# Kernel tuning notes

Hardware: AMD Instinct MI355X
Metric: run time of the kernel (lower is better)

Reference implementation:

```python
import jax, jax.numpy as jnp
import numpy as np

EMBED = 2048
HEADS = 32
HEAD_DIM = EMBED // HEADS
ALPHA = 12.0
MAX_SEQ = 1024
GAMMA = -ALPHA / MAX_SEQ  # clipped softmax lower stretch
ETA = 1.0


def setup_inputs() -> dict:
    key = jax.random.key(0)
    ks = jax.random.split(key, 12)
    B, T, E, H, D = 4, 1024, EMBED, HEADS, HEAD_DIM
    s = 1.0 / np.sqrt(E)
    hidden_states = jax.random.normal(ks[0], (B, T, E), dtype=jnp.float32)
    # causal attention mask: True = attend
    causal = jnp.tril(jnp.ones((T, T), dtype=bool))
    attention_mask = jnp.broadcast_to(causal[None, None], (B, 1, T, T))
    Wq = jax.random.normal(ks[1], (E, E), dtype=jnp.float32) * s
    bq = jnp.zeros((E,), dtype=jnp.float32)
    Wk = jax.random.normal(ks[2], (E, E), dtype=jnp.float32) * s
    bk = jnp.zeros((E,), dtype=jnp.float32)
    Wv = jax.random.normal(ks[3], (E, E), dtype=jnp.float32) * s
    bv = jnp.zeros((E,), dtype=jnp.float32)
    Wo = jax.random.normal(ks[4], (E, E), dtype=jnp.float32) * s
    bo = jnp.zeros((E,), dtype=jnp.float32)
    gate_w = jax.random.normal(ks[5], (H, D), dtype=jnp.float32) * (1.0 / np.sqrt(D))
    gate_b = jnp.zeros((H,), dtype=jnp.float32)
    return {"hidden_states": hidden_states, "attention_mask": attention_mask,
            "Wq": Wq, "bq": bq, "Wk": Wk, "bk": bk, "Wv": Wv, "bv": bv,
            "Wo": Wo, "bo": bo, "gate_w": gate_w, "gate_b": gate_b}


def clipped_softmax(x, gamma, eta):
    p = jax.nn.softmax(x, axis=-1)
    return jnp.clip((eta - gamma) * p + gamma, 0.0, 1.0)


def reference(hidden_states, attention_mask, Wq, bq, Wk, bk, Wv, bv, Wo, bo, gate_w, gate_b):
    B, T, E = hidden_states.shape
    H, D = HEADS, HEAD_DIM
    scaling = D ** -0.5
    neg_min = jnp.finfo(hidden_states.dtype).min

    q = ((hidden_states @ Wq.T + bq) * scaling).reshape(B, T, H, D)
    k = (hidden_states @ Wk.T + bk).reshape(B, T, H, D)
    v = (hidden_states @ Wv.T + bv).reshape(B, T, H, D)

    # scores: [B,H,T,S]
    scores = jnp.einsum('bthd,bshd->bhts', q, k)
    mask_add = jnp.where(attention_mask, 0.0, neg_min)  # [B,1,T,S]
    scores = jnp.maximum(scores + mask_add, neg_min)

    probs = clipped_softmax(scores, GAMMA, ETA)

    attn_out = jnp.einsum('bhts,bshd->bhtd', probs, v)  # [B,H,T,D]

    # conditional_per_token gate: per-head Linear(head_dim -> 1), sigmoid
    x_heads = hidden_states.reshape(B, T, H, D)
    gate = jax.nn.sigmoid(jnp.einsum('bthd,hd->bht', x_heads, gate_w) + gate_b[None, :, None])
    attn_out = attn_out * gate[..., None]  # gate_scaling_factor = 1.0

    out = attn_out.transpose(0, 2, 1, 3).reshape(B, T, E)
    return out @ Wo.T + bo
```

## Files before the change

kernel.cpp:

```cpp
#include <hip/hip_runtime.h>
#include <hip/hip_bf16.h>

typedef unsigned short ushort_t;
using short8 = __attribute__((ext_vector_type(8))) short;
using f32x4  = __attribute__((ext_vector_type(4))) float;

constexpr int B_ = 4;
constexpr int T_ = 1024;
constexpr int E_ = 2048;
constexpr int H_ = 32;
constexpr int D_ = 64;
constexpr float GAMMA_  = -12.0f / 1024.0f;
constexpr float ONE_MG_ = 1.0f - GAMMA_;

__device__ __forceinline__ ushort_t f2bf(float f) {
  union { float f; unsigned int i; } x; x.f = f;
  unsigned int u = x.i;
  u += 0x7fffu + ((u >> 16) & 1u);
  return (ushort_t)(u >> 16);
}

__global__ __launch_bounds__(256) void f2bf_multi(
    const float* __restrict__ x,
    const float* __restrict__ Wq, const float* __restrict__ Wk,
    const float* __restrict__ Wv, const float* __restrict__ Wo,
    ushort_t* __restrict__ xb,
    ushort_t* __restrict__ wqb, ushort_t* __restrict__ wkb,
    ushort_t* __restrict__ wvb, ushort_t* __restrict__ wob) {
  const int i = blockIdx.x * 256 + threadIdx.x;
  const float* src; ushort_t* dst; int off;
  if (i < 2097152)      { src = x;  dst = xb;  off = i; }
  else if (i < 3145728) { src = Wq; dst = wqb; off = i - 2097152; }
  else if (i < 4194304) { src = Wk; dst = wkb; off = i - 3145728; }
  else if (i < 5242880) { src = Wv; dst = wvb; off = i - 4194304; }
  else                  { src = Wo; dst = wob; off = i - 5242880; }
  const float4 f = ((const float4*)src)[off];
  ushort4 u; u.x = f2bf(f.x); u.y = f2bf(f.y); u.z = f2bf(f.z); u.w = f2bf(f.w);
  ((ushort4*)dst)[off] = u;
}

__device__ __forceinline__ void gl_lds16(const ushort_t* g, ushort_t* l) {
  __builtin_amdgcn_global_load_lds(
      (const __attribute__((address_space(1))) void*)g,
      (__attribute__((address_space(3))) void*)l, 16, 0, 0);
}

__global__ __launch_bounds__(256) void gemm_qkv(
    const ushort_t* __restrict__ xb,
    const ushort_t* __restrict__ wq, const ushort_t* __restrict__ wk,
    const ushort_t* __restrict__ wv,
    const float* __restrict__ bq, const float* __restrict__ bk,
    const float* __restrict__ bv,
    ushort_t* __restrict__ qout, ushort_t* __restrict__ kout,
    ushort_t* __restrict__ vtout) {
  constexpr int K = 2048;
  __shared__ ushort_t As[128 * 32];
  __shared__ ushort_t Bs[128 * 32];
  const int which = blockIdx.x >> 4;
  const int colt  = blockIdx.x & 15;
  const ushort_t* Wt  = (which == 0) ? wq : (which == 1) ? wk : wv;
  const float*   bias = (which == 0) ? bq : (which == 1) ? bk : bv;
  const float    scale = (which == 0) ? 0.125f : 1.0f;

  const int tid = threadIdx.x;
  const int wave = tid >> 6, lane = tid & 63;
  const int lane15 = lane & 15, quad = lane >> 4;
  const int row0 = blockIdx.y * 128, col0 = colt * 128;
  const int srow = lane >> 2;
  const int scol = (lane & 3) * 8;
  const ushort_t* Ag0 = xb + (size_t)(row0 + wave * 32 + srow) * K + scol;
  const ushort_t* Ag1 = Ag0 + 16 * (size_t)K;
  const ushort_t* Bg0 = Wt + (size_t)(col0 + wave * 32 + srow) * K + scol;
  const ushort_t* Bg1 = Bg0 + 16 * (size_t)K;
  ushort_t* Al0 = &As[(wave * 32     ) * 32];
  ushort_t* Al1 = &As[(wave * 32 + 16) * 32];
  ushort_t* Bl0 = &Bs[(wave * 32     ) * 32];
  ushort_t* Bl1 = &Bs[(wave * 32 + 16) * 32];
  const int wr = wave >> 1, wc = wave & 1;
  const int q8 = quad * 8;

  f32x4 acc[4][4];
#pragma unroll
  for (int i = 0; i < 4; i++)
#pragma unroll
    for (int j = 0; j < 4; j++) acc[i][j] = (f32x4){0.f, 0.f, 0.f, 0.f};

  for (int k0 = 0; k0 < K; k0 += 32) {
    __syncthreads();
    gl_lds16(Ag0 + k0, Al0);
    gl_lds16(Ag1 + k0, Al1);
    gl_lds16(Bg0 + k0, Bl0);
    gl_lds16(Bg1 + k0, Bl1);
    __syncthreads();
    short8 a_f[4], b_f[4];
#pragma unroll
    for (int i = 0; i < 4; i++)
      a_f[i] = *(const short8*)&As[(wr * 64 + i * 16 + lane15) * 32 + q8];
#pragma unroll
    for (int j = 0; j < 4; j++)
      b_f[j] = *(const short8*)&Bs[(wc * 64 + j * 16 + lane15) * 32 + q8];
#pragma unroll
    for (int i = 0; i < 4; i++)
#pragma unroll
      for (int j = 0; j < 4; j++)
        acc[i][j] = __builtin_amdgcn_mfma_f32_16x16x32_bf16(
            a_f[i], b_f[j], acc[i][j], 0, 0, 0);
  }

  ushort_t* outp = (which == 0) ? qout : (which == 1) ? kout : vtout;
#pragma unroll
  for (int j = 0; j < 4; j++) {
    const int c = col0 + wc * 64 + j * 16 + lane15;
    const float bia = bias[c];
#pragma unroll
    for (int i = 0; i < 4; i++) {
#pragma unroll
      for (int reg = 0; reg < 4; reg++) {
        const int r = row0 + wr * 64 + i * 16 + quad * 4 + reg;
        const float val = (acc[i][j][reg] + bia) * scale;
        const int b = r >> 10, t = r & 1023, h = c >> 6, d = c & 63;
        if (which < 2)
          outp[(((size_t)(b * 32 + h)) * 1024 + t) * 64 + d] = f2bf(val);
        else
          outp[(((size_t)(b * 32 + h)) * 64 + d) * 1024 + t] = f2bf(val);
      }
    }
  }
}

__global__ __launch_bounds__(256) void gemm_out(
    const ushort_t* __restrict__ A, const ushort_t* __restrict__ Wt,
    const float* __restrict__ bias, float* __restrict__ Cout) {
  constexpr int K = 2048;
  __shared__ ushort_t As[128 * 32];
  __shared__ ushort_t Bs[128 * 32];
  const int tid = threadIdx.x;
  const int wave = tid >> 6, lane = tid & 63;
  const int lane15 = lane & 15, quad = lane >> 4;
  const int row0 = blockIdx.y * 128, col0 = blockIdx.x * 128;
  const int srow = lane >> 2;
  const int scol = (lane & 3) * 8;
  const ushort_t* Ag0 = A  + (size_t)(row0 + wave * 32 + srow) * K + scol;
  const ushort_t* Ag1 = Ag0 + 16 * (size_t)K;
  const ushort_t* Bg0 = Wt + (size_t)(col0 + wave * 32 + srow) * K + scol;
  const ushort_t* Bg1 = Bg0 + 16 * (size_t)K;
  ushort_t* Al0 = &As[(wave * 32     ) * 32];
  ushort_t* Al1 = &As[(wave * 32 + 16) * 32];
  ushort_t* Bl0 = &Bs[(wave * 32     ) * 32];
  ushort_t* Bl1 = &Bs[(wave * 32 + 16) * 32];
  const int wr = wave >> 1, wc = wave & 1;
  const int q8 = quad * 8;

  f32x4 acc[4][4];
#pragma unroll
  for (int i = 0; i < 4; i++)
#pragma unroll
    for (int j = 0; j < 4; j++) acc[i][j] = (f32x4){0.f, 0.f, 0.f, 0.f};

  for (int k0 = 0; k0 < K; k0 += 32) {
    __syncthreads();
    gl_lds16(Ag0 + k0, Al0);
    gl_lds16(Ag1 + k0, Al1);
    gl_lds16(Bg0 + k0, Bl0);
    gl_lds16(Bg1 + k0, Bl1);
    __syncthreads();
    short8 a_f[4], b_f[4];
#pragma unroll
    for (int i = 0; i < 4; i++)
      a_f[i] = *(const short8*)&As[(wr * 64 + i * 16 + lane15) * 32 + q8];
#pragma unroll
    for (int j = 0; j < 4; j++)
      b_f[j] = *(const short8*)&Bs[(wc * 64 + j * 16 + lane15) * 32 + q8];
#pragma unroll
    for (int i = 0; i < 4; i++)
#pragma unroll
      for (int j = 0; j < 4; j++)
        acc[i][j] = __builtin_amdgcn_mfma_f32_16x16x32_bf16(
            a_f[i], b_f[j], acc[i][j], 0, 0, 0);
  }

#pragma unroll
  for (int j = 0; j < 4; j++) {
    const int c = col0 + wc * 64 + j * 16 + lane15;
    const float bia = bias[c];
#pragma unroll
    for (int i = 0; i < 4; i++) {
#pragma unroll
      for (int reg = 0; reg < 4; reg++) {
        const int r = row0 + wr * 64 + i * 16 + quad * 4 + reg;
        Cout[(size_t)r * 2048 + c] = acc[i][j][reg] + bia;
      }
    }
  }
}

__global__ __launch_bounds__(256) void gates_kernel(
    const float* __restrict__ x, const float* __restrict__ gw,
    const float* __restrict__ gb, float* __restrict__ gates) {
  const int idx = blockIdx.x * 256 + threadIdx.x;
  const int h = idx & 31;
  const int bt = idx >> 5;
  const float* xp = x + (size_t)bt * E_ + h * D_;
  const float* wp = gw + h * D_;
  float s = 0.f;
#pragma unroll
  for (int d = 0; d < D_; d += 4) {
    const float4 xv = *(const float4*)&xp[d];
    const float4 wv = *(const float4*)&wp[d];
    s = fmaf(xv.x, wv.x, s); s = fmaf(xv.y, wv.y, s);
    s = fmaf(xv.z, wv.z, s); s = fmaf(xv.w, wv.w, s);
  }
  s += gb[h];
  gates[idx] = 1.0f / (1.0f + __expf(-s));
}

__global__ __launch_bounds__(256) void attn_mfma(
    const ushort_t* __restrict__ q, const ushort_t* __restrict__ k,
    const ushort_t* __restrict__ vt, const float* __restrict__ gates,
    ushort_t* __restrict__ attn_out) {
  __shared__ ushort_t Kt[64 * 72];
  __shared__ ushort_t Vt[64 * 72];
  __shared__ ushort_t Pb[4][16 * 72];

  const int tid = threadIdx.x;
  const int wave = tid >> 6, lane = tid & 63;
  const int l15 = lane & 15, quad = lane >> 4;
  const int bx = blockIdx.x;
  const int qt = 7 - (bx >> 7);
  const int bh = bx & 127;
  const int h = bh & 31, b = bh >> 5;
  const int t0 = qt * 128;
  const int qt8 = qt * 8;
  const ushort_t* qbase = q  + (size_t)bh * (T_ * D_);
  const ushort_t* kbase = k  + (size_t)bh * (T_ * D_);
  const ushort_t* vbase = vt + (size_t)bh * (D_ * T_);

  short8 qf[2][2];
#pragma unroll
  for (int s = 0; s < 2; s++) {
    const ushort_t* qp =
        qbase + (size_t)(t0 + s * 64 + wave * 16 + l15) * 64 + quad * 8;
    qf[s][0] = *(const short8*)qp;
    qf[s][1] = *(const short8*)(qp + 32);
  }

  const int srow = tid >> 2;
  const int scol = (tid & 3) * 16;
  const int nkt = 2 * qt + 2;

  float l_part[2][4] = {};

  for (int kt = 0; kt < nkt; kt++) {
    __syncthreads();
    {
      const ushort_t* kg = &kbase[(size_t)(kt * 64 + srow) * 64 + scol];
      ushort_t* kl = &Kt[srow * 72 + scol];
      *(short8*)kl = *(const short8*)kg;
      *(short8*)(kl + 8) = *(const short8*)(kg + 8);
    }
    __syncthreads();
#pragma unroll
    for (int s = 0; s < 2; s++) {
      const int rb = qt8 + s * 4 + wave;
      if (kt * 4 > rb) continue;
      f32x4 sc[4];
#pragma unroll
      for (int j = 0; j < 4; j++) {
        const int cb = kt * 4 + j;
        if (cb > rb) {
          sc[j] = (f32x4){-3.0e38f, -3.0e38f, -3.0e38f, -3.0e38f};
          continue;
        }
        const ushort_t* kp = &Kt[(j * 16 + l15) * 72 + quad * 8];
        const short8 kf0 = *(const short8*)kp;
        const short8 kf1 = *(const short8*)(kp + 32);
        f32x4 z = (f32x4){0.f, 0.f, 0.f, 0.f};
        z = __builtin_amdgcn_mfma_f32_16x16x32_bf16(qf[s][0], kf0, z, 0, 0, 0);
        z = __builtin_amdgcn_mfma_f32_16x16x32_bf16(qf[s][1], kf1, z, 0, 0, 0);
        if (cb == rb) {
#pragma unroll
          for (int r = 0; r < 4; r++)
            if (l15 > quad * 4 + r) z[r] = -3.0e38f;
        }
        sc[j] = z;
      }
#pragma unroll
      for (int r = 0; r < 4; r++)
        l_part[s][r] += __expf(sc[0][r]) + __expf(sc[1][r]) +
                        __expf(sc[2][r]) + __expf(sc[3][r]);
    }
  }

  float c1[2][4];
#pragma unroll
  for (int s = 0; s < 2; s++)
#pragma unroll
    for (int r = 0; r < 4; r++) {
      float e = l_part[s][r];
      e += __shfl_xor(e, 1); e += __shfl_xor(e, 2);
      e += __shfl_xor(e, 4); e += __shfl_xor(e, 8);
      c1[s][r] = ONE_MG_ / e;
    }

  f32x4 acc[2][4];
#pragma unroll
  for (int s = 0; s < 2; s++)
#pragma unroll
    for (int jd = 0; jd < 4; jd++) acc[s][jd] = (f32x4){0.f, 0.f, 0.f, 0.f};

  for (int kt = 0; kt < nkt; kt++) {
    __syncthreads();
    {
      const ushort_t* kg = &kbase[(size_t)(kt * 64 + srow) * 64 + scol];
      ushort_t* kl = &Kt[srow * 72 + scol];
      *(short8*)kl = *(const short8*)kg;
      *(short8*)(kl + 8) = *(const short8*)(kg + 8);
      const ushort_t* vg = &vbase[(size_t)srow * 1024 + kt * 64 + scol];
      ushort_t* vl = &Vt[srow * 72 + scol];
      *(short8*)vl = *(const short8*)vg;
      *(short8*)(vl + 8) = *(const short8*)(vg + 8);
    }
    __syncthreads();
#pragma unroll
    for (int s = 0; s < 2; s++) {
      const int rb = qt8 + s * 4 + wave;
      if (kt * 4 > rb) continue;
      f32x4 sc[4];
#pragma unroll
      for (int j = 0; j < 4; j++) {
        const int cb = kt * 4 + j;
        if (cb > rb) {
          sc[j] = (f32x4){-3.0e38f, -3.0e38f, -3.0e38f, -3.0e38f};
          continue;
        }
        const ushort_t* kp = &Kt[(j * 16 + l15) * 72 + quad * 8];
        const short8 kf0 = *(const short8*)kp;
        const short8 kf1 = *(const short8*)(kp + 32);
        f32x4 z = (f32x4){0.f, 0.f, 0.f, 0.f};
        z = __builtin_amdgcn_mfma_f32_16x16x32_bf16(qf[s][0], kf0, z, 0, 0, 0);
        z = __builtin_amdgcn_mfma_f32_16x16x32_bf16(qf[s][1], kf1, z, 0, 0, 0);
        if (cb == rb) {
#pragma unroll
          for (int r = 0; r < 4; r++)
            if (l15 > quad * 4 + r) z[r] = -3.0e38f;
        }
        sc[j] = z;
      }
      ushort_t* pb = &Pb[wave][0];
#pragma unroll
      for (int j = 0; j < 4; j++) {
#pragma unroll
        for (int r = 0; r < 4; r++) {
          float p = fmaf(c1[s][r], __expf(sc[j][r]), GAMMA_);
          p = fminf(fmaxf(p, 0.f), 1.f);
          pb[(quad * 4 + r) * 72 + j * 16 + l15] = f2bf(p);
        }
      }
      const short8 pf0 = *(const short8*)&pb[l15 * 72 + quad * 8];
      const short8 pf1 = *(const short8*)&pb[l15 * 72 + 32 + quad * 8];
#pragma unroll
      for (int jd = 0; jd < 4; jd++) {
        const ushort_t* vp = &Vt[(jd * 16 + l15) * 72 + quad * 8];
        const short8 vf0 = *(const short8*)vp;
        const short8 vf1 = *(const short8*)(vp + 32);
        acc[s][jd] =
            __builtin_amdgcn_mfma_f32_16x16x32_bf16(pf0, vf0, acc[s][jd], 0, 0, 0);
        acc[s][jd] =
            __builtin_amdgcn_mfma_f32_16x16x32_bf16(pf1, vf1, acc[s][jd], 0, 0, 0);
      }
    }
  }

#pragma unroll
  for (int s = 0; s < 2; s++) {
#pragma unroll
    for (int r = 0; r < 4; r++) {
      const int t = t0 + s * 64 + wave * 16 + quad * 4 + r;
      const float g = gates[((size_t)b * T_ + t) * H_ + h];
      ushort_t* op = attn_out + ((size_t)b * T_ + t) * E_ + h * 64;
#pragma unroll
      for (int jd = 0; jd < 4; jd++)
        op[jd * 16 + l15] = f2bf(acc[s][jd][r] * g);
    }
  }
}

extern "C" void kernel_launch(void* const* d_in, const int* in_sizes, int n_in,
                              void* d_out, int out_size, void* d_ws, size_t ws_size,
                              hipStream_t stream) {
  (void)in_sizes; (void)n_in; (void)out_size; (void)ws_size;
  const float* x  = (const float*)d_in[0];
  const float* Wq = (const float*)d_in[2];
  const float* bq = (const float*)d_in[3];
  const float* Wk = (const float*)d_in[4];
  const float* bk = (const float*)d_in[5];
  const float* Wv = (const float*)d_in[6];
  const float* bv = (const float*)d_in[7];
  const float* Wo = (const float*)d_in[8];
  const float* bo = (const float*)d_in[9];
  const float* gw = (const float*)d_in[10];
  const float* gb = (const float*)d_in[11];
  float* out = (float*)d_out;

  char* W = (char*)d_ws;
  ushort_t* xb  = (ushort_t*)(W + 0);
  ushort_t* wqb = (ushort_t*)(W + 16777216);
  ushort_t* wkb = (ushort_t*)(W + 25165824);
  ushort_t* wvb = (ushort_t*)(W + 33554432);
  ushort_t* wob = (ushort_t*)(W + 41943040);
  ushort_t* qb  = (ushort_t*)(W + 50331648);
  ushort_t* kb  = (ushort_t*)(W + 67108864);
  ushort_t* vtb = (ushort_t*)(W + 83886080);
  ushort_t* ab  = (ushort_t*)(W + 100663296);
  float*    gts = (float*)(W + 117440512);

  f2bf_multi<<<24576, 256, 0, stream>>>(x, Wq, Wk, Wv, Wo,
                                        xb, wqb, wkb, wvb, wob);

  gemm_qkv<<<dim3(48, 32), 256, 0, stream>>>(xb, wqb, wkb, wvb,
                                             bq, bk, bv, qb, kb, vtb);
  gates_kernel<<<512, 256, 0, stream>>>(x, gw, gb, gts);
  attn_mfma<<<1024, 256, 0, stream>>>(qb, kb, vtb, gts, ab);
  gemm_out<<<dim3(16, 32), 256, 0, stream>>>(ab, wob, bo, out);
}
```

Before: 435.1 us.

## Replace QKV and output GEMMs with a pipelined 256x256 tile core

Both GEMMs move from a 128x128 tile with a single LDS buffer and two barriers per 32-wide k step to a shared 256x256 core with 8 waves. The core double-buffers 64-wide k slices in XOR-swizzled LDS and issues global-to-LDS loads for upcoming slices between four MFMA quadrant phases, using s_setprio and explicit vmcnt waits. It also remaps block indices to improve L2 reuse. The goal is to hide memory latency, cut LDS bank conflicts and raise MFMA utilisation. The trade-offs are far fewer blocks (128 for the output GEMM, which is under one full wave on the CU count), more register and LDS pressure, and more barriers per iteration.

Result: slower. 449.4 us (+3.3%).

```diff
diff --git a/kernel.cpp b/kernel.cpp
--- a/kernel.cpp
+++ b/kernel.cpp
@@ -45,7 +45,128 @@
       (__attribute__((address_space(3))) void*)l, 16, 0, 0);
 }
 
-__global__ __launch_bounds__(256) void gemm_qkv(
+
+__device__ __forceinline__ void stage_half(
+    const ushort_t* __restrict__ g, int grow0, int k0,
+    ushort_t* l, int wid, int lane) {
+  const int rl = lane >> 3;
+  const int c7 = (lane & 7) ^ rl;
+#pragma unroll
+  for (int q = 0; q < 2; q++) {
+    const ushort_t* src =
+        g + (size_t)(grow0 + (q * 8 + wid) * 8 + rl) * 2048 + k0 + c7 * 8;
+    gl_lds16(src, l + (q * 8 + wid) * 512);
+  }
+}
+
+__device__ __forceinline__ void ld_a(short8 (&a)[8], const ushort_t* base,
+                                     int wm, int l15, int sw0, int sw1) {
+#pragma unroll
+  for (int m = 0; m < 4; m++) {
+    const ushort_t* p = base + (wm * 64 + m * 16 + l15) * 64;
+    a[m * 2 + 0] = *(const short8*)(p + sw0);
+    a[m * 2 + 1] = *(const short8*)(p + sw1);
+  }
+}
+
+__device__ __forceinline__ void ld_b(short8 (&b)[4], const ushort_t* base,
+                                     int wn, int l15, int sw0, int sw1) {
+#pragma unroll
+  for (int n = 0; n < 2; n++) {
+    const ushort_t* p = base + (wn * 32 + n * 16 + l15) * 64;
+    b[n * 2 + 0] = *(const short8*)(p + sw0);
+    b[n * 2 + 1] = *(const short8*)(p + sw1);
+  }
+}
+
+template <int QM, int QN>
+__device__ __forceinline__ void mfma_phase(f32x4 (&acc)[8][4],
+                                           const short8 (&a)[8],
+                                           const short8 (&bfr)[4]) {
+#pragma unroll
+  for (int m = 0; m < 4; m++)
+#pragma unroll
+    for (int n = 0; n < 2; n++)
+#pragma unroll
+      for (int kc = 0; kc < 2; kc++)
+        acc[QM * 4 + m][QN * 2 + n] = __builtin_amdgcn_mfma_f32_16x16x32_bf16(
+            a[m * 2 + kc], bfr[n * 2 + kc], acc[QM * 4 + m][QN * 2 + n],
+            0, 0, 0);
+}
+
+#define GFENCE asm volatile("" ::: "memory")
+
+__device__ __forceinline__ void gemm256_core(
+    const ushort_t* __restrict__ Ag, const ushort_t* __restrict__ Bg,
+    const int row0, const int col0,
+    ushort_t (&lds)[2][2][2][8192], f32x4 (&acc)[8][4]) {
+  const int tid = threadIdx.x;
+  const int wid = tid >> 6, lane = tid & 63;
+  const int wm = wid >> 2, wn = wid & 3;
+  const int l15 = lane & 15, quad = lane >> 4;
+  const int sw0 = (quad * 8) ^ ((l15 & 7) << 3);
+  const int sw1 = (32 + quad * 8) ^ ((l15 & 7) << 3);
+
+#pragma unroll
+  for (int i = 0; i < 8; i++)
+#pragma unroll
+    for (int j = 0; j < 4; j++) acc[i][j] = (f32x4){0.f, 0.f, 0.f, 0.f};
+
+  short8 a[8], bfr[4];
+
+  stage_half(Ag, row0,       0,  &lds[0][0][0][0], wid, lane);
+  stage_half(Bg, col0 + 128, 0,  &lds[0][1][1][0], wid, lane);
+  stage_half(Ag, row0 + 128, 0,  &lds[0][0][1][0], wid, lane);
+  stage_half(Bg, col0,       0,  &lds[0][1][0][0], wid, lane);
+  stage_half(Ag, row0,       64, &lds[1][0][0][0], wid, lane);
+  stage_half(Bg, col0 + 128, 64, &lds[1][1][1][0], wid, lane);
+  stage_half(Ag, row0 + 128, 64, &lds[1][0][1][0], wid, lane);
+  asm volatile("s_waitcnt vmcnt(6)" ::: "memory");
+  __builtin_amdgcn_s_barrier();
+  GFENCE;
+
+  for (int t = 0; t < 32; ++t) {
+    const int buf = t & 1;
+    const int kf = (t + 2) * 64;
+    ld_a(a, &lds[buf][0][0][0], wm, l15, sw0, sw1);
+    ld_b(bfr, &lds[buf][1][0][0], wn, l15, sw0, sw1);
+    if (t + 1 < 32)
+      stage_half(Bg, col0, (t + 1) * 64, &lds[buf ^ 1][1][0][0], wid, lane);
+    GFENCE; __builtin_amdgcn_s_barrier(); GFENCE;
+    __builtin_amdgcn_s_setprio(1);
+    mfma_phase<0, 0>(acc, a, bfr);
+    __builtin_amdgcn_s_setprio(0);
+    GFENCE; __builtin_amdgcn_s_barrier(); GFENCE;
+    ld_b(bfr, &lds[buf][1][1][0], wn, l15, sw0, sw1);
+    if (t + 2 < 32)
+      stage_half(Ag, row0, kf, &lds[buf][0][0][0], wid, lane);
+    GFENCE; __builtin_amdgcn_s_barrier(); GFENCE;
+    __builtin_amdgcn_s_setprio(1);
+    mfma_phase<0, 1>(acc, a, bfr);
+    __builtin_amdgcn_s_setprio(0);
+    GFENCE; __builtin_amdgcn_s_barrier(); GFENCE;
+    ld_a(a, &lds[buf][0][1][0], wm, l15, sw0, sw1);
+    if (t + 2 < 32)
+      stage_half(Bg, col0 + 128, kf, &lds[buf][1][1][0], wid, lane);
+    GFENCE; __builtin_amdgcn_s_barrier(); GFENCE;
+    __builtin_amdgcn_s_setprio(1);
+    mfma_phase<1, 1>(acc, a, bfr);
+    __builtin_amdgcn_s_setprio(0);
+    GFENCE; __builtin_amdgcn_s_barrier(); GFENCE;
+    ld_b(bfr, &lds[buf][1][0][0], wn, l15, sw0, sw1);
+    if (t + 2 < 32)
+      stage_half(Ag, row0 + 128, kf, &lds[buf][0][1][0], wid, lane);
+    GFENCE; __builtin_amdgcn_s_barrier(); GFENCE;
+    __builtin_amdgcn_s_setprio(1);
+    mfma_phase<1, 0>(acc, a, bfr);
+    __builtin_amdgcn_s_setprio(0);
+    if (t < 30)       asm volatile("s_waitcnt vmcnt(6)" ::: "memory");
+    else if (t == 30) asm volatile("s_waitcnt vmcnt(0)" ::: "memory");
+    GFENCE; __builtin_amdgcn_s_barrier(); GFENCE;
+  }
+}
+
+__global__ __launch_bounds__(512, 2) void gemm_qkv256(
     const ushort_t* __restrict__ xb,
     const ushort_t* __restrict__ wq, const ushort_t* __restrict__ wk,
     const ushort_t* __restrict__ wv,
@@ -53,143 +174,73 @@
     const float* __restrict__ bv,
     ushort_t* __restrict__ qout, ushort_t* __restrict__ kout,
     ushort_t* __restrict__ vtout) {
-  constexpr int K = 2048;
-  __shared__ ushort_t As[128 * 32];
-  __shared__ ushort_t Bs[128 * 32];
-  const int which = blockIdx.x >> 4;
-  const int colt  = blockIdx.x & 15;
+  __shared__ ushort_t lds[2][2][2][8192];
+  const int g = blockIdx.x;
+  const int swz = (g & 7) * 48 + (g >> 3);
+  const int which = swz >> 7;
+  const int rem = swz & 127;
+  const int row0 = (rem & 15) * 256;
+  const int col0 = (rem >> 4) * 256;
   const ushort_t* Wt  = (which == 0) ? wq : (which == 1) ? wk : wv;
   const float*   bias = (which == 0) ? bq : (which == 1) ? bk : bv;
   const float    scale = (which == 0) ? 0.125f : 1.0f;
+  ushort_t* outp = (which == 0) ? qout : (which == 1) ? kout : vtout;
+
+  f32x4 acc[8][4];
+  gemm256_core(xb, Wt, row0, col0, lds, acc);
 
   const int tid = threadIdx.x;
-  const int wave = tid >> 6, lane = tid & 63;
-  const int lane15 = lane & 15, quad = lane >> 4;
-  const int row0 = blockIdx.y * 128, col0 = colt * 128;
-  const int srow = lane >> 2;
-  const int scol = (lane & 3) * 8;
-  const ushort_t* Ag0 = xb + (size_t)(row0 + wave * 32 + srow) * K + scol;
-  const ushort_t* Ag1 = Ag0 + 16 * (size_t)K;
-  const ushort_t* Bg0 = Wt + (size_t)(col0 + wave * 32 + srow) * K + scol;
-  const ushort_t* Bg1 = Bg0 + 16 * (size_t)K;
-  ushort_t* Al0 = &As[(wave * 32     ) * 32];
-  ushort_t* Al1 = &As[(wave * 32 + 16) * 32];
-  ushort_t* Bl0 = &Bs[(wave * 32     ) * 32];
-  ushort_t* Bl1 = &Bs[(wave * 32 + 16) * 32];
-  const int wr = wave >> 1, wc = wave & 1;
-  const int q8 = quad * 8;
-
-  f32x4 acc[4][4];
-#pragma unroll
-  for (int i = 0; i < 4; i++)
-#pragma unroll
-    for (int j = 0; j < 4; j++) acc[i][j] = (f32x4){0.f, 0.f, 0.f, 0.f};
-
-  for (int k0 = 0; k0 < K; k0 += 32) {
-    __syncthreads();
-    gl_lds16(Ag0 + k0, Al0);
-    gl_lds16(Ag1 + k0, Al1);
-    gl_lds16(Bg0 + k0, Bl0);
-    gl_lds16(Bg1 + k0, Bl1);
-    __syncthreads();
-    short8 a_f[4], b_f[4];
-#pragma unroll
-    for (int i = 0; i < 4; i++)
-      a_f[i] = *(const short8*)&As[(wr * 64 + i * 16 + lane15) * 32 + q8];
-#pragma unroll
-    for (int j = 0; j < 4; j++)
-      b_f[j] = *(const short8*)&Bs[(wc * 64 + j * 16 + lane15) * 32 + q8];
-#pragma unroll
-    for (int i = 0; i < 4; i++)
-#pragma unroll
-      for (int j = 0; j < 4; j++)
-        acc[i][j] = __builtin_amdgcn_mfma_f32_16x16x32_bf16(
-            a_f[i], b_f[j], acc[i][j], 0, 0, 0);
-  }
-
-  ushort_t* outp = (which == 0) ? qout : (which == 1) ? kout : vtout;
-#pragma unroll
-  for (int j = 0; j < 4; j++) {
-    const int c = col0 + wc * 64 + j * 16 + lane15;
-    const float bia = bias[c];
-#pragma unroll
-    for (int i = 0; i < 4; i++) {
+  const int wid = tid >> 6, lane = tid & 63;
+  const int wm = wid >> 2, wn = wid & 3;
+  const int l15 = lane & 15, quad = lane >> 4;
+#pragma unroll
+  for (int ai = 0; ai < 8; ai++) {
+    const int r0 = row0 + (ai >> 2) * 128 + wm * 64 + (ai & 3) * 16 + quad * 4;
+#pragma unroll
+    for (int aj = 0; aj < 4; aj++) {
+      const int c = col0 + (aj >> 1) * 128 + wn * 32 + (aj & 1) * 16 + l15;
+      const float bia = bias[c];
+      const int h = c >> 6, d = c & 63;
 #pragma unroll
       for (int reg = 0; reg < 4; reg++) {
-        const int r = row0 + wr * 64 + i * 16 + quad * 4 + reg;
-        const float val = (acc[i][j][reg] + bia) * scale;
-        const int b = r >> 10, t = r & 1023, h = c >> 6, d = c & 63;
+        const int rr = r0 + reg;
+        const float val = (acc[ai][aj][reg] + bia) * scale;
+        const int b = rr >> 10, tt = rr & 1023;
         if (which < 2)
-          outp[(((size_t)(b * 32 + h)) * 1024 + t) * 64 + d] = f2bf(val);
+          outp[(((size_t)(b * 32 + h)) * 1024 + tt) * 64 + d] = f2bf(val);
         else
-          outp[(((size_t)(b * 32 + h)) * 64 + d) * 1024 + t] = f2bf(val);
+          outp[(((size_t)(b * 32 + h)) * 64 + d) * 1024 + tt] = f2bf(val);
       }
     }
   }
 }
 
-__global__ __launch_bounds__(256) void gemm_out(
+__global__ __launch_bounds__(512, 2) void gemm_out256(
     const ushort_t* __restrict__ A, const ushort_t* __restrict__ Wt,
     const float* __restrict__ bias, float* __restrict__ Cout) {
-  constexpr int K = 2048;
-  __shared__ ushort_t As[128 * 32];
-  __shared__ ushort_t Bs[128 * 32];
+  __shared__ ushort_t lds[2][2][2][8192];
+  const int g = blockIdx.x;
+  const int swz = (g & 7) * 16 + (g >> 3);
+  const int row0 = (swz & 15) * 256;
+  const int col0 = (swz >> 4) * 256;
+
+  f32x4 acc[8][4];
+  gemm256_core(A, Wt, row0, col0, lds, acc);
+
   const int tid = threadIdx.x;
-  const int wave = tid >> 6, lane = tid & 63;
-  const int lane15 = lane & 15, quad = lane >> 4;
-  const int row0 = blockIdx.y * 128, col0 = blockIdx.x * 128;
-  const int srow = lane >> 2;
-  const int scol = (lane & 3) * 8;
-  const ushort_t* Ag0 = A  + (size_t)(row0 + wave * 32 + srow) * K + scol;
-  const ushort_t* Ag1 = Ag0 + 16 * (size_t)K;
-  const ushort_t* Bg0 = Wt + (size_t)(col0 + wave * 32 + srow) * K + scol;
-  const ushort_t* Bg1 = Bg0 + 16 * (size_t)K;
-  ushort_t* Al0 = &As[(wave * 32     ) * 32];
-  ushort_t* Al1 = &As[(wave * 32 + 16) * 32];
-  ushort_t* Bl0 = &Bs[(wave * 32     ) * 32];
-  ushort_t* Bl1 = &Bs[(wave * 32 + 16) * 32];
-  const int wr = wave >> 1, wc = wave & 1;
-  const int q8 = quad * 8;
-
-  f32x4 acc[4][4];
-#pragma unroll
-  for (int i = 0; i < 4; i++)
-#pragma unroll
-    for (int j = 0; j < 4; j++) acc[i][j] = (f32x4){0.f, 0.f, 0.f, 0.f};
-
-  for (int k0 = 0; k0 < K; k0 += 32) {
-    __syncthreads();
-    gl_lds16(Ag0 + k0, Al0);
-    gl_lds16(Ag1 + k0, Al1);
-    gl_lds16(Bg0 + k0, Bl0);
-    gl_lds16(Bg1 + k0, Bl1);
-    __syncthreads();
-    short8 a_f[4], b_f[4];
-#pragma unroll
-    for (int i = 0; i < 4; i++)
-      a_f[i] = *(const short8*)&As[(wr * 64 + i * 16 + lane15) * 32 + q8];
-#pragma unroll
-    for (int j = 0; j < 4; j++)
-      b_f[j] = *(const short8*)&Bs[(wc * 64 + j * 16 + lane15) * 32 + q8];
-#pragma unroll
-    for (int i = 0; i < 4; i++)
-#pragma unroll
-      for (int j = 0; j < 4; j++)
-        acc[i][j] = __builtin_amdgcn_mfma_f32_16x16x32_bf16(
-            a_f[i], b_f[j], acc[i][j], 0, 0, 0);
-  }
-
-#pragma unroll
-  for (int j = 0; j < 4; j++) {
-    const int c = col0 + wc * 64 + j * 16 + lane15;
-    const float bia = bias[c];
-#pragma unroll
-    for (int i = 0; i < 4; i++) {
-#pragma unroll
-      for (int reg = 0; reg < 4; reg++) {
-        const int r = row0 + wr * 64 + i * 16 + quad * 4 + reg;
-        Cout[(size_t)r * 2048 + c] = acc[i][j][reg] + bia;
-      }
+  const int wid = tid >> 6, lane = tid & 63;
+  const int wm = wid >> 2, wn = wid & 3;
+  const int l15 = lane & 15, quad = lane >> 4;
+#pragma unroll
+  for (int ai = 0; ai < 8; ai++) {
+    const int r0 = row0 + (ai >> 2) * 128 + wm * 64 + (ai & 3) * 16 + quad * 4;
+#pragma unroll
+    for (int aj = 0; aj < 4; aj++) {
+      const int c = col0 + (aj >> 1) * 128 + wn * 32 + (aj & 1) * 16 + l15;
+      const float bia = bias[c];
+#pragma unroll
+      for (int reg = 0; reg < 4; reg++)
+        Cout[(size_t)(r0 + reg) * 2048 + c] = acc[ai][aj][reg] + bia;
     }
   }
 }
@@ -417,9 +468,9 @@
   f2bf_multi<<<24576, 256, 0, stream>>>(x, Wq, Wk, Wv, Wo,
                                         xb, wqb, wkb, wvb, wob);
 
-  gemm_qkv<<<dim3(48, 32), 256, 0, stream>>>(xb, wqb, wkb, wvb,
-                                             bq, bk, bv, qb, kb, vtb);
+  gemm_qkv256<<<384, 512, 0, stream>>>(xb, wqb, wkb, wvb,
+                                       bq, bk, bv, qb, kb, vtb);
   gates_kernel<<<512, 256, 0, stream>>>(x, gw, gb, gts);
   attn_mfma<<<1024, 256, 0, stream>>>(qb, kb, vtb, gts, ab);
-  gemm_out<<<dim3(16, 32), 256, 0, stream>>>(ab, wob, bo, out);
-}
+  gemm_out256<<<128, 512, 0, stream>>>(ab, wob, bo, out);
+}
```

## Load K/V fragments directly from global memory and remap blocks per XCD

Applied to the files above, without the earlier changes.

Removes the shared-memory staging of K and V tiles and the two block-wide barriers per key tile. Each wave now reads its MFMA operand fragments straight from global memory, relying on L2/L1 cache reuse across the four waves. The block index is also remapped so that blocks sharing the same batch-head land on the same XCD, which is meant to improve L2 locality. The trade-off is redundant global loads per wave and longer load latency without LDS reuse.

Result: slower. 467.9 us (+7.5%).

```diff
diff --git a/kernel.cpp b/kernel.cpp
--- a/kernel.cpp
+++ b/kernel.cpp
@@ -218,19 +218,17 @@
     const ushort_t* __restrict__ q, const ushort_t* __restrict__ k,
     const ushort_t* __restrict__ vt, const float* __restrict__ gates,
     ushort_t* __restrict__ attn_out) {
-  __shared__ ushort_t Kt[64 * 72];
-  __shared__ ushort_t Vt[64 * 72];
   __shared__ ushort_t Pb[4][16 * 72];
 
   const int tid = threadIdx.x;
   const int wave = tid >> 6, lane = tid & 63;
   const int l15 = lane & 15, quad = lane >> 4;
   const int bx = blockIdx.x;
-  const int qt = 7 - (bx >> 7);
-  const int bh = bx & 127;
+  const int xcd = bx & 7, w = bx >> 3;
+  const int bh = xcd * 16 + (w & 15);
+  const int qt = 7 - (w >> 4);
   const int h = bh & 31, b = bh >> 5;
   const int t0 = qt * 128;
-  const int qt8 = qt * 8;
   const ushort_t* qbase = q  + (size_t)bh * (T_ * D_);
   const ushort_t* kbase = k  + (size_t)bh * (T_ * D_);
   const ushort_t* vbase = vt + (size_t)bh * (D_ * T_);
@@ -244,36 +242,32 @@
     qf[s][1] = *(const short8*)(qp + 32);
   }
 
-  const int srow = tid >> 2;
-  const int scol = (tid & 3) * 16;
   const int nkt = 2 * qt + 2;
+  const int rb0 = qt * 8 + wave;
+  const int rb1 = qt * 8 + 4 + wave;
 
   float l_part[2][4] = {};
 
   for (int kt = 0; kt < nkt; kt++) {
-    __syncthreads();
-    {
-      const ushort_t* kg = &kbase[(size_t)(kt * 64 + srow) * 64 + scol];
-      ushort_t* kl = &Kt[srow * 72 + scol];
-      *(short8*)kl = *(const short8*)kg;
-      *(short8*)(kl + 8) = *(const short8*)(kg + 8);
-    }
-    __syncthreads();
-#pragma unroll
-    for (int s = 0; s < 2; s++) {
-      const int rb = qt8 + s * 4 + wave;
-      if (kt * 4 > rb) continue;
-      f32x4 sc[4];
-#pragma unroll
-      for (int j = 0; j < 4; j++) {
-        const int cb = kt * 4 + j;
+    f32x4 sc[2][4];
+#pragma unroll
+    for (int j = 0; j < 4; j++) {
+      const int cb = kt * 4 + j;
+      if (cb > rb1) {
+        sc[0][j] = sc[1][j] = (f32x4){-3.0e38f, -3.0e38f, -3.0e38f, -3.0e38f};
+        continue;
+      }
+      const ushort_t* kp =
+          kbase + (size_t)(kt * 64 + j * 16 + l15) * 64 + quad * 8;
+      const short8 kf0 = *(const short8*)kp;
+      const short8 kf1 = *(const short8*)(kp + 32);
+#pragma unroll
+      for (int s = 0; s < 2; s++) {
+        const int rb = s ? rb1 : rb0;
         if (cb > rb) {
-          sc[j] = (f32x4){-3.0e38f, -3.0e38f, -3.0e38f, -3.0e38f};
+          sc[s][j] = (f32x4){-3.0e38f, -3.0e38f, -3.0e38f, -3.0e38f};
           continue;
         }
-        const ushort_t* kp = &Kt[(j * 16 + l15) * 72 + quad * 8];
-        const short8 kf0 = *(const short8*)kp;
-        const short8 kf1 = *(const short8*)(kp + 32);
         f32x4 z = (f32x4){0.f, 0.f, 0.f, 0.f};
         z = __builtin_amdgcn_mfma_f32_16x16x32_bf16(qf[s][0], kf0, z, 0, 0, 0);
         z = __builtin_amdgcn_mfma_f32_16x16x32_bf16(qf[s][1], kf1, z, 0, 0, 0);
@@ -282,12 +276,16 @@
           for (int r = 0; r < 4; r++)
             if (l15 > quad * 4 + r) z[r] = -3.0e38f;
         }
-        sc[j] = z;
-      }
+        sc[s][j] = z;
+      }
+    }
+#pragma unroll
+    for (int s = 0; s < 2; s++) {
+      if (kt * 4 > (s ? rb1 : rb0)) continue;
 #pragma unroll
       for (int r = 0; r < 4; r++)
-        l_part[s][r] += __expf(sc[0][r]) + __expf(sc[1][r]) +
-                        __expf(sc[2][r]) + __expf(sc[3][r]);
+        l_part[s][r] += __expf(sc[s][0][r]) + __expf(sc[s][1][r]) +
+                        __expf(sc[s][2][r]) + __expf(sc[s][3][r]);
     }
   }
 
@@ -309,33 +307,25 @@
     for (int jd = 0; jd < 4; jd++) acc[s][jd] = (f32x4){0.f, 0.f, 0.f, 0.f};
 
   for (int kt = 0; kt < nkt; kt++) {
-    __syncthreads();
-    {
-      const ushort_t* kg = &kbase[(size_t)(kt * 64 + srow) * 64 + scol];
-      ushort_t* kl = &Kt[srow * 72 + scol];
-      *(short8*)kl = *(const short8*)kg;
-      *(short8*)(kl + 8) = *(const short8*)(kg + 8);
-      const ushort_t* vg = &vbase[(size_t)srow * 1024 + kt * 64 + scol];
-      ushort_t* vl = &Vt[srow * 72 + scol];
-      *(short8*)vl = *(const short8*)vg;
-      *(short8*)(vl + 8) = *(const short8*)(vg + 8);
-    }
-    __syncthreads();
-#pragma unroll
-    for (int s = 0; s < 2; s++) {
-      const int rb = qt8 + s * 4 + wave;
-      if (kt * 4 > rb) continue;
-      f32x4 sc[4];
-#pragma unroll
-      for (int j = 0; j < 4; j++) {
-        const int cb = kt * 4 + j;
+    f32x4 sc[2][4];
+#pragma unroll
+    for (int j = 0; j < 4; j++) {
+      const int cb = kt * 4 + j;
+      if (cb > rb1) {
+        sc[0][j] = sc[1][j] = (f32x4){-3.0e38f, -3.0e38f, -3.0e38f, -3.0e38f};
+        continue;
+      }
+      const ushort_t* kp =
+          kbase + (size_t)(kt * 64 + j * 16 + l15) * 64 + quad * 8;
+      const short8 kf0 = *(const short8*)kp;
+      const short8 kf1 = *(const short8*)(kp + 32);
+#pragma unroll
+      for (int s = 0; s < 2; s++) {
+        const int rb = s ? rb1 : rb0;
         if (cb > rb) {
-          sc[j] = (f32x4){-3.0e38f, -3.0e38f, -3.0e38f, -3.0e38f};
+          sc[s][j] = (f32x4){-3.0e38f, -3.0e38f, -3.0e38f, -3.0e38f};
           continue;
         }
-        const ushort_t* kp = &Kt[(j * 16 + l15) * 72 + quad * 8];
-        const short8 kf0 = *(const short8*)kp;
-        const short8 kf1 = *(const short8*)(kp + 32);
         f32x4 z = (f32x4){0.f, 0.f, 0.f, 0.f};
         z = __builtin_amdgcn_mfma_f32_16x16x32_bf16(qf[s][0], kf0, z, 0, 0, 0);
         z = __builtin_amdgcn_mfma_f32_16x16x32_bf16(qf[s][1], kf1, z, 0, 0, 0);
@@ -344,30 +334,43 @@
           for (int r = 0; r < 4; r++)
             if (l15 > quad * 4 + r) z[r] = -3.0e38f;
         }
-        sc[j] = z;
-      }
+        sc[s][j] = z;
+      }
+    }
+    short8 pf[2][2];
+#pragma unroll
+    for (int s = 0; s < 2; s++) {
+      if (kt * 4 > (s ? rb1 : rb0)) continue;
       ushort_t* pb = &Pb[wave][0];
 #pragma unroll
       for (int j = 0; j < 4; j++) {
 #pragma unroll
         for (int r = 0; r < 4; r++) {
-          float p = fmaf(c1[s][r], __expf(sc[j][r]), GAMMA_);
+          float p = fmaf(c1[s][r], __expf(sc[s][j][r]), GAMMA_);
           p = fminf(fmaxf(p, 0.f), 1.f);
           pb[(quad * 4 + r) * 72 + j * 16 + l15] = f2bf(p);
         }
       }
-      const short8 pf0 = *(const short8*)&pb[l15 * 72 + quad * 8];
-      const short8 pf1 = *(const short8*)&pb[l15 * 72 + 32 + quad * 8];
-#pragma unroll
-      for (int jd = 0; jd < 4; jd++) {
-        const ushort_t* vp = &Vt[(jd * 16 + l15) * 72 + quad * 8];
-        const short8 vf0 = *(const short8*)vp;
-        const short8 vf1 = *(const short8*)(vp + 32);
-        acc[s][jd] =
-            __builtin_amdgcn_mfma_f32_16x16x32_bf16(pf0, vf0, acc[s][jd], 0, 0, 0);
-        acc[s][jd] =
-            __builtin_amdgcn_mfma_f32_16x16x32_bf16(pf1, vf1, acc[s][jd], 0, 0, 0);
-      }
+      pf[s][0] = *(const short8*)&pb[l15 * 72 + quad * 8];
+      pf[s][1] = *(const short8*)&pb[l15 * 72 + 32 + quad * 8];
+    }
+    const bool do0 = (kt * 4 <= rb0);
+#pragma unroll
+    for (int jd = 0; jd < 4; jd++) {
+      const ushort_t* vp =
+          vbase + (size_t)(jd * 16 + l15) * 1024 + kt * 64 + quad * 8;
+      const short8 vf0 = *(const short8*)vp;
+      const short8 vf1 = *(const short8*)(vp + 32);
+      if (do0) {
+        acc[0][jd] =
+            __builtin_amdgcn_mfma_f32_16x16x32_bf16(pf[0][0], vf0, acc[0][jd], 0, 0, 0);
+        acc[0][jd] =
+            __builtin_amdgcn_mfma_f32_16x16x32_bf16(pf[0][1], vf1, acc[0][jd], 0, 0, 0);
+      }
+      acc[1][jd] =
+          __builtin_amdgcn_mfma_f32_16x16x32_bf16(pf[1][0], vf0, acc[1][jd], 0, 0, 0);
+      acc[1][jd] =
+          __builtin_amdgcn_mfma_f32_16x16x32_bf16(pf[1][1], vf1, acc[1][jd], 0, 0, 0);
     }
   }
 
```

## Double-buffer K/V tiles in attention with register prefetch of next tile

Applied to the files above, without the earlier changes.

The attention kernel now keeps two LDS buffers for K and V. Each loop iteration issues global loads for the next tile into registers, runs the MFMA work on the current buffer, then writes the prefetched tile into the other buffer. This cuts the two barriers per iteration to one and hides global load latency behind compute. The cost is double the LDS for K/V and extra live registers, which may lower occupancy.

Result: faster. 424.6 us (-2.4%).

```diff
diff --git a/kernel.cpp b/kernel.cpp
--- a/kernel.cpp
+++ b/kernel.cpp
@@ -218,8 +218,8 @@
     const ushort_t* __restrict__ q, const ushort_t* __restrict__ k,
     const ushort_t* __restrict__ vt, const float* __restrict__ gates,
     ushort_t* __restrict__ attn_out) {
-  __shared__ ushort_t Kt[64 * 72];
-  __shared__ ushort_t Vt[64 * 72];
+  __shared__ ushort_t Kt[2][64 * 72];
+  __shared__ ushort_t Vt[2][64 * 72];
   __shared__ ushort_t Pb[4][16 * 72];
 
   const int tid = threadIdx.x;
@@ -250,15 +250,23 @@
 
   float l_part[2][4] = {};
 
+  {
+    const ushort_t* kg = &kbase[(size_t)srow * 64 + scol];
+    const short8 k0 = *(const short8*)kg;
+    const short8 k1 = *(const short8*)(kg + 8);
+    ushort_t* kl = &Kt[0][srow * 72 + scol];
+    *(short8*)kl = k0; *(short8*)(kl + 8) = k1;
+  }
+  __syncthreads();
   for (int kt = 0; kt < nkt; kt++) {
-    __syncthreads();
-    {
-      const ushort_t* kg = &kbase[(size_t)(kt * 64 + srow) * 64 + scol];
-      ushort_t* kl = &Kt[srow * 72 + scol];
-      *(short8*)kl = *(const short8*)kg;
-      *(short8*)(kl + 8) = *(const short8*)(kg + 8);
-    }
-    __syncthreads();
+    const int buf = kt & 1;
+    const bool more = (kt + 1 < nkt);
+    short8 nk0, nk1;
+    if (more) {
+      const ushort_t* kg = &kbase[(size_t)((kt + 1) * 64 + srow) * 64 + scol];
+      nk0 = *(const short8*)kg;
+      nk1 = *(const short8*)(kg + 8);
+    }
 #pragma unroll
     for (int s = 0; s < 2; s++) {
       const int rb = qt8 + s * 4 + wave;
@@ -271,7 +279,7 @@
           sc[j] = (f32x4){-3.0e38f, -3.0e38f, -3.0e38f, -3.0e38f};
           continue;
         }
-        const ushort_t* kp = &Kt[(j * 16 + l15) * 72 + quad * 8];
+        const ushort_t* kp = &Kt[buf][(j * 16 + l15) * 72 + quad * 8];
         const short8 kf0 = *(const short8*)kp;
         const short8 kf1 = *(const short8*)(kp + 32);
         f32x4 z = (f32x4){0.f, 0.f, 0.f, 0.f};
@@ -289,6 +297,11 @@
         l_part[s][r] += __expf(sc[0][r]) + __expf(sc[1][r]) +
                         __expf(sc[2][r]) + __expf(sc[3][r]);
     }
+    if (more) {
+      ushort_t* kl = &Kt[buf ^ 1][srow * 72 + scol];
+      *(short8*)kl = nk0; *(short8*)(kl + 8) = nk1;
+      __syncthreads();
+    }
   }
 
   float c1[2][4];
@@ -308,19 +321,32 @@
 #pragma unroll
     for (int jd = 0; jd < 4; jd++) acc[s][jd] = (f32x4){0.f, 0.f, 0.f, 0.f};
 
+  __syncthreads();
+  {
+    const ushort_t* kg = &kbase[(size_t)srow * 64 + scol];
+    const short8 k0 = *(const short8*)kg;
+    const short8 k1 = *(const short8*)(kg + 8);
+    ushort_t* kl = &Kt[0][srow * 72 + scol];
+    *(short8*)kl = k0; *(short8*)(kl + 8) = k1;
+    const ushort_t* vg = &vbase[(size_t)srow * 1024 + scol];
+    const short8 v0 = *(const short8*)vg;
+    const short8 v1 = *(const short8*)(vg + 8);
+    ushort_t* vl = &Vt[0][srow * 72 + scol];
+    *(short8*)vl = v0; *(short8*)(vl + 8) = v1;
+  }
+  __syncthreads();
   for (int kt = 0; kt < nkt; kt++) {
-    __syncthreads();
-    {
-      const ushort_t* kg = &kbase[(size_t)(kt * 64 + srow) * 64 + scol];
-      ushort_t* kl = &Kt[srow * 72 + scol];
-      *(short8*)kl = *(const short8*)kg;
-      *(short8*)(kl + 8) = *(const short8*)(kg + 8);
-      const ushort_t* vg = &vbase[(size_t)srow * 1024 + kt * 64 + scol];
-      ushort_t* vl = &Vt[srow * 72 + scol];
-      *(short8*)vl = *(const short8*)vg;
-      *(short8*)(vl + 8) = *(const short8*)(vg + 8);
-    }
-    __syncthreads();
+    const int buf = kt & 1;
+    const bool more = (kt + 1 < nkt);
+    short8 nk0, nk1, nv0, nv1;
+    if (more) {
+      const ushort_t* kg = &kbase[(size_t)((kt + 1) * 64 + srow) * 64 + scol];
+      nk0 = *(const short8*)kg;
+      nk1 = *(const short8*)(kg + 8);
+      const ushort_t* vg = &vbase[(size_t)srow * 1024 + (kt + 1) * 64 + scol];
+      nv0 = *(const short8*)vg;
+      nv1 = *(const short8*)(vg + 8);
+    }
 #pragma unroll
     for (int s = 0; s < 2; s++) {
       const int rb = qt8 + s * 4 + wave;
@@ -333,7 +359,7 @@
           sc[j] = (f32x4){-3.0e38f, -3.0e38f, -3.0e38f, -3.0e38f};
           continue;
         }
-        const ushort_t* kp = &Kt[(j * 16 + l15) * 72 + quad * 8];
+        const ushort_t* kp = &Kt[buf][(j * 16 + l15) * 72 + quad * 8];
         const short8 kf0 = *(const short8*)kp;
         const short8 kf1 = *(const short8*)(kp + 32);
         f32x4 z = (f32x4){0.f, 0.f, 0.f, 0.f};
@@ -360,7 +386,7 @@
       const short8 pf1 = *(const short8*)&pb[l15 * 72 + 32 + quad * 8];
 #pragma unroll
       for (int jd = 0; jd < 4; jd++) {
-        const ushort_t* vp = &Vt[(jd * 16 + l15) * 72 + quad * 8];
+        const ushort_t* vp = &Vt[buf][(jd * 16 + l15) * 72 + quad * 8];
         const short8 vf0 = *(const short8*)vp;
         const short8 vf1 = *(const short8*)(vp + 32);
         acc[s][jd] =
@@ -368,6 +394,13 @@
         acc[s][jd] =
             __builtin_amdgcn_mfma_f32_16x16x32_bf16(pf1, vf1, acc[s][jd], 0, 0, 0);
       }
+    }
+    if (more) {
+      ushort_t* kl = &Kt[buf ^ 1][srow * 72 + scol];
+      *(short8*)kl = nk0; *(short8*)(kl + 8) = nk1;
+      ushort_t* vl = &Vt[buf ^ 1][srow * 72 + scol];
+      *(short8*)vl = nv0; *(short8*)(vl + 8) = nv1;
+      __syncthreads();
     }
   }
 
```
